# Kernel tuning notes

Measured on AMD Instinct MI355X. Metric: run time of the kernel, lower is better.

Reference implementation:

```python
import jax, jax.numpy as jnp
import numpy as np
from math import sqrt

NUM_HEADS = 8
HIDDEN = 768
ATTN_DIM = HIDDEN // NUM_HEADS  # 96
NEG = -1e10


def setup_inputs() -> dict:
    key = jax.random.key(0)
    ks = jax.random.split(key, 6)
    b, s, dim = 8, 1024, 768
    scale = 1.0 / sqrt(dim)
    return {
        "span_embeddings": jax.random.normal(ks[0], (b, s, dim), dtype=jnp.float32),
        "span_tags": jax.random.randint(ks[1], (b, s), 0, 5),
        "w_weight": jax.random.normal(ks[2], (1, dim), dtype=jnp.float32) * scale,
        "w_q": jax.random.normal(ks[3], (HIDDEN, dim), dtype=jnp.float32) * scale,
        "w_k": jax.random.normal(ks[4], (HIDDEN, dim), dtype=jnp.float32) * scale,
        "w_v": jax.random.normal(ks[5], (HIDDEN, dim), dtype=jnp.float32) * scale,
    }


def reference(span_embeddings, span_tags, w_weight, w_q, w_k, w_v):
    b, s, _ = span_embeddings.shape
    pad = span_tags == 0  # [b, s]

    # additive span attention weights: Linear(dim -> 1), mask padded, softmax over seq
    attn_weights = span_embeddings @ w_weight.T  # [b, s, 1]
    attn_weights = jnp.where(pad[:, :, None], NEG, attn_weights)
    attn_weights = jax.nn.softmax(attn_weights, axis=1)

    # NOTE: original views hidden as (attn_dim, num_heads) in that order
    qs = (span_embeddings @ w_q.T).reshape(b, s, ATTN_DIM, NUM_HEADS)
    ks = (span_embeddings @ w_k.T).reshape(b, s, ATTN_DIM, NUM_HEADS)
    vs = (span_embeddings @ w_v.T).reshape(b, s, ATTN_DIM, NUM_HEADS)

    rel = jnp.einsum('bqdh,bkdh->bqkh', qs, ks) / sqrt(ATTN_DIM)  # [b,q,k,h]
    # original masks along query axis (relevance_weights[span_tags.eq(0)] = NEG)
    rel = jnp.where(pad[:, :, None, None], NEG, rel)
    # original softmax(dim=-1) -> over the HEADS axis (faithful quirk)
    rel = jax.nn.softmax(rel, axis=-1)

    span_value = jnp.einsum('bqkh,bkdh->bqdh', rel, vs).reshape(b, s, HIDDEN)
    weighted_value = jnp.sum(attn_weights * span_value, axis=1)  # [b, hidden]
    return weighted_value
```

## Files before the change

kernel.cpp:

```cpp
#include <hip/hip_runtime.h>
#include <hip/hip_bf16.h>
#include <math.h>

#define NEGV (-1e10f)

typedef __attribute__((ext_vector_type(8))) short bf16x8;
typedef __attribute__((ext_vector_type(4))) float f32x4;
typedef __attribute__((ext_vector_type(16))) float f32x16;

static __device__ __forceinline__ unsigned short f2bf(float f) {
  unsigned int u = __builtin_bit_cast(unsigned int, f);
  unsigned int r = (u + 0x7fffu + ((u >> 16) & 1u)) >> 16;
  return (unsigned short)r;
}
static __device__ __forceinline__ float bf2f(unsigned short v) {
  return __builtin_bit_cast(float, (unsigned int)v << 16);
}

#define GLD16(g, l)                                                   \
  __builtin_amdgcn_global_load_lds(                                   \
      (const __attribute__((address_space(1))) void*)(g),             \
      (__attribute__((address_space(3))) void*)(l), 16, 0, 0)

__global__ __launch_bounds__(256) void cast_emb_logits(
    const float* __restrict__ emb, const int* __restrict__ tags,
    const float* __restrict__ ww, unsigned short* __restrict__ embbf,
    float* __restrict__ logits) {
  int w = threadIdx.x >> 6, lane = threadIdx.x & 63;
  int row = blockIdx.x * 4 + w;
  const float4* src = (const float4*)(emb + (size_t)row * 768);
  const float4* wsrc = (const float4*)ww;
  ushort4* dst = (ushort4*)(embbf + (size_t)row * 768);
  float d = 0.f;
#pragma unroll
  for (int j = 0; j < 3; j++) {
    int idx = lane + 64 * j;
    float4 v = src[idx];
    float4 wv = wsrc[idx];
    d += v.x * wv.x + v.y * wv.y + v.z * wv.z + v.w * wv.w;
    ushort4 o;
    o.x = f2bf(v.x); o.y = f2bf(v.y); o.z = f2bf(v.z); o.w = f2bf(v.w);
    dst[idx] = o;
  }
#pragma unroll
  for (int off = 32; off; off >>= 1) d += __shfl_xor(d, off);
  if (lane == 0) logits[row] = (tags[row] == 0) ? NEGV : d;
}

__global__ __launch_bounds__(256) void cast_w(
    const float* __restrict__ wq, const float* __restrict__ wk,
    const float* __restrict__ wv, unsigned short* __restrict__ out) {
  int z = blockIdx.y;
  const float* src = (z == 0) ? wq : (z == 1) ? wk : wv;
  int idx = blockIdx.x * 256 + threadIdx.x;
  float4 v = ((const float4*)src)[idx];
  ushort4 o;
  o.x = f2bf(v.x); o.y = f2bf(v.y); o.z = f2bf(v.z); o.w = f2bf(v.w);
  ((ushort4*)(out + (size_t)z * 589824))[idx] = o;
}

__global__ __launch_bounds__(256) void softmax_aw(
    const float* __restrict__ logits, float* __restrict__ aw) {
  __shared__ float red[4];
  int b = blockIdx.x, t = threadIdx.x;
  const float* L = logits + b * 1024;
  float x0 = L[t], x1 = L[t + 256], x2 = L[t + 512], x3 = L[t + 768];
  float m = fmaxf(fmaxf(x0, x1), fmaxf(x2, x3));
#pragma unroll
  for (int off = 32; off; off >>= 1) m = fmaxf(m, __shfl_xor(m, off));
  if ((t & 63) == 0) red[t >> 6] = m;
  __syncthreads();
  m = fmaxf(fmaxf(red[0], red[1]), fmaxf(red[2], red[3]));
  float e0 = __expf(x0 - m), e1 = __expf(x1 - m), e2 = __expf(x2 - m),
        e3 = __expf(x3 - m);
  float s = e0 + e1 + e2 + e3;
#pragma unroll
  for (int off = 32; off; off >>= 1) s += __shfl_xor(s, off);
  __syncthreads();
  if ((t & 63) == 0) red[t >> 6] = s;
  __syncthreads();
  float inv = 1.0f / (red[0] + red[1] + red[2] + red[3]);
  float* A = aw + b * 1024;
  A[t] = e0 * inv; A[t + 256] = e1 * inv;
  A[t + 512] = e2 * inv; A[t + 768] = e3 * inv;
}

__global__ __launch_bounds__(256) void qkv_gemm(
    const unsigned short* __restrict__ A, const unsigned short* __restrict__ Wbf,
    unsigned short* __restrict__ Qf, unsigned short* __restrict__ Kf,
    unsigned short* __restrict__ Vbf) {
  __shared__ __align__(16) unsigned short sm[16640];
  unsigned short* As = sm;
  unsigned short* Bs = sm + 8192;
  int z = blockIdx.z;
  const unsigned short* B = Wbf + (size_t)z * 589824;
  int mb = blockIdx.x * 128, nb = blockIdx.y * 128;
  int tid = threadIdx.x;
  int w = tid >> 6, lane = tid & 63;
  int wm = w >> 1, wn = w & 1;
  int c = lane & 15, quad = lane >> 4;
  int lrow = lane >> 2, lcol = (lane & 3) * 8;
  const unsigned short* Ag = A + (size_t)(mb + w * 32 + lrow) * 768 + lcol;
  const unsigned short* Bg = B + (size_t)(nb + w * 32 + lrow) * 768 + lcol;
  int woff = w * 1024;

#define PREFETCH(buf, kb)                                              \
  do {                                                                 \
    GLD16(Ag + (kb), As + (buf) * 4096 + woff);                        \
    GLD16(Ag + (kb) + 16 * 768, As + (buf) * 4096 + woff + 512);       \
    GLD16(Bg + (kb), Bs + (buf) * 4096 + woff);                        \
    GLD16(Bg + (kb) + 16 * 768, Bs + (buf) * 4096 + woff + 512);       \
  } while (0)

  f32x4 acc[4][4];
#pragma unroll
  for (int i = 0; i < 4; i++)
#pragma unroll
    for (int j = 0; j < 4; j++) acc[i][j] = 0;

  PREFETCH(0, 0);
  for (int it = 0; it < 24; it++) {
    __syncthreads();
    if (it + 1 < 24) PREFETCH((it + 1) & 1, (it + 1) * 32);
    const unsigned short* Ab = As + (it & 1) * 4096;
    const unsigned short* Bb = Bs + (it & 1) * 4096;
    bf16x8 af[4], bfr[4];
#pragma unroll
    for (int i = 0; i < 4; i++)
      af[i] = *(const bf16x8*)&Ab[(wm * 64 + i * 16 + c) * 32 + quad * 8];
#pragma unroll
    for (int j = 0; j < 4; j++)
      bfr[j] = *(const bf16x8*)&Bb[(wn * 64 + j * 16 + c) * 32 + quad * 8];
#pragma unroll
    for (int i = 0; i < 4; i++)
#pragma unroll
      for (int j = 0; j < 4; j++)
        acc[i][j] = __builtin_amdgcn_mfma_f32_16x16x32_bf16(af[i], bfr[j],
                                                            acc[i][j], 0, 0, 0);
  }
  __syncthreads();

  if (z == 2) {
#pragma unroll
    for (int i = 0; i < 4; i++)
#pragma unroll
      for (int j = 0; j < 4; j++)
#pragma unroll
        for (int r = 0; r < 4; r++) {
          int rowg = mb + wm * 64 + i * 16 + quad * 4 + r;
          int colg = nb + wn * 64 + j * 16 + c;
          Vbf[(size_t)rowg * 768 + colg] = f2bf(acc[i][j][r]);
        }
  } else {
    unsigned short* O = (z == 0) ? Qf : Kf;
#pragma unroll
    for (int i = 0; i < 4; i++) {
#pragma unroll
      for (int j = 0; j < 4; j++) {
#pragma unroll
        for (int r = 0; r < 4; r++) {
          int ql = wm * 64 + i * 16 + quad * 4 + r;
          int h = c & 7;
          int elem = j * 2 + (c >> 3);
          int chunkL = (ql >> 5) * 8 + h;
          int lane32 = (ql & 31) + wn * 32;
          sm[chunkL * 520 + lane32 * 8 + elem] = f2bf(acc[i][j][r]);
        }
      }
    }
    __syncthreads();
    int bq = mb >> 10;
    int qt32g0 = (mb & 1023) >> 5;
    int tt = blockIdx.y;
#pragma unroll
    for (int it2 = 0; it2 < 8; it2++) {
      int g = it2 * 256 + tid;
      int chunkL = g >> 6;
      int off = (g & 63) * 8;
      bf16x8 vdat = *(const bf16x8*)&sm[chunkL * 520 + off];
      int qt32 = qt32g0 + (chunkL >> 3), h = chunkL & 7;
      size_t dst = ((((size_t)(bq * 32 + qt32) * 8 + h) * 6 + tt) << 9) + off;
      *(bf16x8*)&O[dst] = vdat;
    }
  }
#undef PREFETCH
}

__global__ __launch_bounds__(256) void attn(
    const unsigned short* __restrict__ Qf, const unsigned short* __restrict__ Kf,
    const float* __restrict__ aw, float* __restrict__ Ptp) {
  __shared__ __align__(16) unsigned short Qs[2 * 6144];
  __shared__ __align__(16) unsigned short Ks[2 * 6144];
  __shared__ float pbuf[1024];
  int b = blockIdx.z, qb = blockIdx.y, kb = blockIdx.x;
  int tid = threadIdx.x, w = tid >> 6, lane = tid & 63;
  int wq = w >> 1, wk = w & 1;

#define STAGE(hh, buf)                                                        \
  do {                                                                        \
    _Pragma("unroll") for (int call = 0; call < 3; call++) {                  \
      int cc = call * 4 + w;                                                  \
      int qt32 = (cc >= 6) ? 1 : 0;                                           \
      int t5 = cc - qt32 * 6;                                                 \
      size_t go = ((((size_t)(b * 32 + qb * 2 + qt32) * 8 + (hh)) * 6 + t5)   \
                   << 9) + lane * 8;                                          \
      size_t ko = ((((size_t)(b * 32 + kb * 2 + qt32) * 8 + (hh)) * 6 + t5)   \
                   << 9) + lane * 8;                                          \
      GLD16(Qf + go, Qs + (buf) * 6144 + cc * 512);                           \
      GLD16(Kf + ko, Ks + (buf) * 6144 + cc * 512);                           \
    }                                                                         \
  } while (0)

  f32x16 acc[8];
#pragma unroll
  for (int h = 0; h < 8; h++) acc[h] = 0;

  STAGE(0, 0);
#pragma unroll
  for (int h = 0; h < 8; h++) {
    __syncthreads();
    if (h + 1 < 8) STAGE(h + 1, (h + 1) & 1);
    const unsigned short* Qb = Qs + (h & 1) * 6144;
    const unsigned short* Kb = Ks + (h & 1) * 6144;
#pragma unroll
    for (int t = 0; t < 6; t++) {
      bf16x8 a = *(const bf16x8*)&Qb[(wq * 6 + t) * 512 + lane * 8];
      bf16x8 bb = *(const bf16x8*)&Kb[(wk * 6 + t) * 512 + lane * 8];
      acc[h] = __builtin_amdgcn_mfma_f32_32x32x16_bf16(a, bb, acc[h], 0, 0, 0);
    }
  }

  float awv[16];
#pragma unroll
  for (int reg = 0; reg < 16; reg++) {
    int row = (reg & 3) + 8 * (reg >> 2) + 4 * (lane >> 5);
    awv[reg] = aw[b * 1024 + qb * 64 + wq * 32 + row];
  }
  float partial[8];
#pragma unroll
  for (int h = 0; h < 8; h++) partial[h] = 0.f;
  const float C2 = 0.10206207261596577f * 1.4426950408889634f;
#pragma unroll
  for (int reg = 0; reg < 16; reg++) {
    float v[8], m = -1e30f;
#pragma unroll
    for (int h = 0; h < 8; h++) {
      v[h] = acc[h][reg] * C2;
      m = fmaxf(m, v[h]);
    }
    float ssum = 0.f;
#pragma unroll
    for (int h = 0; h < 8; h++) {
      float e = exp2f(v[h] - m);
      v[h] = e;
      ssum += e;
    }
    float g = awv[reg] * __builtin_amdgcn_rcpf(ssum);
#pragma unroll
    for (int h = 0; h < 8; h++) partial[h] += v[h] * g;
  }
#pragma unroll
  for (int h = 0; h < 8; h++) {
    float v = partial[h];
    v += __shfl_xor(v, 32);
    partial[h] = v;
  }
  if (lane < 32) {
#pragma unroll
    for (int h = 0; h < 8; h++) pbuf[w * 256 + lane * 8 + h] = partial[h];
  }
  __syncthreads();
#pragma unroll
  for (int wk2 = 0; wk2 < 2; wk2++) {
    float s = pbuf[wk2 * 256 + tid] + pbuf[(2 + wk2) * 256 + tid];
    int kcol = tid >> 3, h = tid & 7;
    Ptp[(((size_t)qb * 8 + b) * 1024 + kb * 64 + wk2 * 32 + kcol) * 8 + h] = s;
  }
#undef STAGE
}

__global__ __launch_bounds__(256) void finalize(
    const float* __restrict__ Ptp, const unsigned short* __restrict__ Vbf,
    float* __restrict__ out) {
  __shared__ float ps[256];
  int kc = blockIdx.x, b = blockIdx.y;
  int t = threadIdx.x;
  {
    int k = kc * 32 + (t >> 3), h = t & 7;
    float s = 0.f;
#pragma unroll
    for (int qc = 0; qc < 16; qc++)
      s += Ptp[(((size_t)qc * 8 + b) * 1024 + k) * 8 + h];
    ps[t] = s;
  }
  __syncthreads();
  int h = t & 7;
  float a0 = 0, a1 = 0, a2 = 0;
  const unsigned short* Vb = Vbf + ((size_t)b * 1024 + kc * 32) * 768;
#pragma unroll 4
  for (int kk = 0; kk < 32; kk++) {
    float p = ps[kk * 8 + h];
    const unsigned short* vr = Vb + (size_t)kk * 768;
    a0 += p * bf2f(vr[t]);
    a1 += p * bf2f(vr[t + 256]);
    a2 += p * bf2f(vr[t + 512]);
  }
  atomicAdd(&out[b * 768 + t], a0);
  atomicAdd(&out[b * 768 + t + 256], a1);
  atomicAdd(&out[b * 768 + t + 512], a2);
}

extern "C" void kernel_launch(void* const* d_in, const int* in_sizes, int n_in,
                              void* d_out, int out_size, void* d_ws,
                              size_t ws_size, hipStream_t stream) {
  const float* emb = (const float*)d_in[0];
  const int* tags = (const int*)d_in[1];
  const float* ww = (const float*)d_in[2];
  const float* wq = (const float*)d_in[3];
  const float* wk = (const float*)d_in[4];
  const float* wv = (const float*)d_in[5];
  float* out = (float*)d_out;
  char* ws = (char*)d_ws;
  unsigned short* embbf = (unsigned short*)(ws + 0);
  unsigned short* wbf   = (unsigned short*)(ws + 12582912);
  unsigned short* Qf    = (unsigned short*)(ws + 16121856);
  unsigned short* Kf    = (unsigned short*)(ws + 28704768);
  unsigned short* Vbf   = (unsigned short*)(ws + 41287680);
  float* logits         = (float*)(ws + 53870592);
  float* aw             = (float*)(ws + 53903360);
  float* Ptp            = (float*)(ws + 53936128);

  hipMemsetAsync(out, 0, 8 * 768 * sizeof(float), stream);
  cast_emb_logits<<<2048, 256, 0, stream>>>(emb, tags, ww, embbf, logits);
  cast_w<<<dim3(576, 3), 256, 0, stream>>>(wq, wk, wv, wbf);
  softmax_aw<<<8, 256, 0, stream>>>(logits, aw);
  qkv_gemm<<<dim3(64, 6, 3), 256, 0, stream>>>(embbf, wbf, Qf, Kf, Vbf);
  attn<<<dim3(16, 16, 8), 256, 0, stream>>>(Qf, Kf, aw, Ptp);
  finalize<<<dim3(32, 8), 256, 0, stream>>>(Ptp, Vbf, out);
}
```

Measured before the change: 188.1 us.

## Merge cast kernels, load attn fragments directly from global, vectorize finalize

Merges the embedding cast/logit kernel and the weight cast kernel into a single launch that dispatches on block index, saving one launch. The attention kernel no longer stages Q/K through double-buffered LDS with barriers; each wave reads its MFMA fragments straight from the pre-tiled global layout, dropping the LDS footprint and syncs but losing cross-wave sharing (each Q/K tile is read twice from global/L2). The finalize kernel loads 4 bf16 values per thread with a vector load and uses 192 active threads instead of 256 doing scalar loads.

```diff
diff --git a/kernel.cpp b/kernel.cpp
--- a/kernel.cpp
+++ b/kernel.cpp
@@ -22,41 +22,43 @@
       (const __attribute__((address_space(1))) void*)(g),             \
       (__attribute__((address_space(3))) void*)(l), 16, 0, 0)
 
-__global__ __launch_bounds__(256) void cast_emb_logits(
+__global__ __launch_bounds__(256) void cast_inputs(
     const float* __restrict__ emb, const int* __restrict__ tags,
-    const float* __restrict__ ww, unsigned short* __restrict__ embbf,
-    float* __restrict__ logits) {
-  int w = threadIdx.x >> 6, lane = threadIdx.x & 63;
-  int row = blockIdx.x * 4 + w;
-  const float4* src = (const float4*)(emb + (size_t)row * 768);
-  const float4* wsrc = (const float4*)ww;
-  ushort4* dst = (ushort4*)(embbf + (size_t)row * 768);
-  float d = 0.f;
-#pragma unroll
-  for (int j = 0; j < 3; j++) {
-    int idx = lane + 64 * j;
-    float4 v = src[idx];
-    float4 wv = wsrc[idx];
-    d += v.x * wv.x + v.y * wv.y + v.z * wv.z + v.w * wv.w;
+    const float* __restrict__ ww, const float* __restrict__ wq,
+    const float* __restrict__ wk, const float* __restrict__ wv,
+    unsigned short* __restrict__ embbf, float* __restrict__ logits,
+    unsigned short* __restrict__ wbf) {
+  int bx = blockIdx.x;
+  if (bx < 2048) {
+    int w = threadIdx.x >> 6, lane = threadIdx.x & 63;
+    int row = bx * 4 + w;
+    const float4* src = (const float4*)(emb + (size_t)row * 768);
+    const float4* wsrc = (const float4*)ww;
+    ushort4* dst = (ushort4*)(embbf + (size_t)row * 768);
+    float d = 0.f;
+#pragma unroll
+    for (int j = 0; j < 3; j++) {
+      int idx = lane + 64 * j;
+      float4 v = src[idx];
+      float4 wv = wsrc[idx];
+      d += v.x * wv.x + v.y * wv.y + v.z * wv.z + v.w * wv.w;
+      ushort4 o;
+      o.x = f2bf(v.x); o.y = f2bf(v.y); o.z = f2bf(v.z); o.w = f2bf(v.w);
+      dst[idx] = o;
+    }
+#pragma unroll
+    for (int off = 32; off; off >>= 1) d += __shfl_xor(d, off);
+    if (lane == 0) logits[row] = (tags[row] == 0) ? NEGV : d;
+  } else {
+    int g = bx - 2048;
+    int z = g / 576;
+    int idx = (g - z * 576) * 256 + threadIdx.x;
+    const float* src = (z == 0) ? wq : (z == 1) ? wk : wv;
+    float4 v = ((const float4*)src)[idx];
     ushort4 o;
     o.x = f2bf(v.x); o.y = f2bf(v.y); o.z = f2bf(v.z); o.w = f2bf(v.w);
-    dst[idx] = o;
-  }
-#pragma unroll
-  for (int off = 32; off; off >>= 1) d += __shfl_xor(d, off);
-  if (lane == 0) logits[row] = (tags[row] == 0) ? NEGV : d;
-}
-
-__global__ __launch_bounds__(256) void cast_w(
-    const float* __restrict__ wq, const float* __restrict__ wk,
-    const float* __restrict__ wv, unsigned short* __restrict__ out) {
-  int z = blockIdx.y;
-  const float* src = (z == 0) ? wq : (z == 1) ? wk : wv;
-  int idx = blockIdx.x * 256 + threadIdx.x;
-  float4 v = ((const float4*)src)[idx];
-  ushort4 o;
-  o.x = f2bf(v.x); o.y = f2bf(v.y); o.z = f2bf(v.z); o.w = f2bf(v.w);
-  ((ushort4*)(out + (size_t)z * 589824))[idx] = o;
+    ((ushort4*)(wbf + (size_t)z * 589824))[idx] = o;
+  }
 }
 
 __global__ __launch_bounds__(256) void softmax_aw(
@@ -189,43 +191,24 @@
 __global__ __launch_bounds__(256) void attn(
     const unsigned short* __restrict__ Qf, const unsigned short* __restrict__ Kf,
     const float* __restrict__ aw, float* __restrict__ Ptp) {
-  __shared__ __align__(16) unsigned short Qs[2 * 6144];
-  __shared__ __align__(16) unsigned short Ks[2 * 6144];
   __shared__ float pbuf[1024];
   int b = blockIdx.z, qb = blockIdx.y, kb = blockIdx.x;
   int tid = threadIdx.x, w = tid >> 6, lane = tid & 63;
   int wq = w >> 1, wk = w & 1;
-
-#define STAGE(hh, buf)                                                        \
-  do {                                                                        \
-    _Pragma("unroll") for (int call = 0; call < 3; call++) {                  \
-      int cc = call * 4 + w;                                                  \
-      int qt32 = (cc >= 6) ? 1 : 0;                                           \
-      int t5 = cc - qt32 * 6;                                                 \
-      size_t go = ((((size_t)(b * 32 + qb * 2 + qt32) * 8 + (hh)) * 6 + t5)   \
-                   << 9) + lane * 8;                                          \
-      size_t ko = ((((size_t)(b * 32 + kb * 2 + qt32) * 8 + (hh)) * 6 + t5)   \
-                   << 9) + lane * 8;                                          \
-      GLD16(Qf + go, Qs + (buf) * 6144 + cc * 512);                           \
-      GLD16(Kf + ko, Ks + (buf) * 6144 + cc * 512);                           \
-    }                                                                         \
-  } while (0)
+  const unsigned short* Qb =
+      Qf + ((size_t)(b * 32 + qb * 2 + wq) * 48) * 512 + (size_t)lane * 8;
+  const unsigned short* Kb =
+      Kf + ((size_t)(b * 32 + kb * 2 + wk) * 48) * 512 + (size_t)lane * 8;
 
   f32x16 acc[8];
 #pragma unroll
   for (int h = 0; h < 8; h++) acc[h] = 0;
-
-  STAGE(0, 0);
 #pragma unroll
   for (int h = 0; h < 8; h++) {
-    __syncthreads();
-    if (h + 1 < 8) STAGE(h + 1, (h + 1) & 1);
-    const unsigned short* Qb = Qs + (h & 1) * 6144;
-    const unsigned short* Kb = Ks + (h & 1) * 6144;
 #pragma unroll
     for (int t = 0; t < 6; t++) {
-      bf16x8 a = *(const bf16x8*)&Qb[(wq * 6 + t) * 512 + lane * 8];
-      bf16x8 bb = *(const bf16x8*)&Kb[(wk * 6 + t) * 512 + lane * 8];
+      bf16x8 a = *(const bf16x8*)(Qb + (size_t)(h * 6 + t) * 512);
+      bf16x8 bb = *(const bf16x8*)(Kb + (size_t)(h * 6 + t) * 512);
       acc[h] = __builtin_amdgcn_mfma_f32_32x32x16_bf16(a, bb, acc[h], 0, 0, 0);
     }
   }
@@ -276,7 +259,6 @@
     int kcol = tid >> 3, h = tid & 7;
     Ptp[(((size_t)qb * 8 + b) * 1024 + kb * 64 + wk2 * 32 + kcol) * 8 + h] = s;
   }
-#undef STAGE
 }
 
 __global__ __launch_bounds__(256) void finalize(
@@ -294,20 +276,25 @@
     ps[t] = s;
   }
   __syncthreads();
-  int h = t & 7;
-  float a0 = 0, a1 = 0, a2 = 0;
-  const unsigned short* Vb = Vbf + ((size_t)b * 1024 + kc * 32) * 768;
+  if (t < 192) {
+    int o0 = t * 4;
+    int hb = o0 & 7;
+    float a0 = 0, a1 = 0, a2 = 0, a3 = 0;
+    const unsigned short* Vb = Vbf + ((size_t)b * 1024 + kc * 32) * 768 + o0;
 #pragma unroll 4
-  for (int kk = 0; kk < 32; kk++) {
-    float p = ps[kk * 8 + h];
-    const unsigned short* vr = Vb + (size_t)kk * 768;
-    a0 += p * bf2f(vr[t]);
-    a1 += p * bf2f(vr[t + 256]);
-    a2 += p * bf2f(vr[t + 512]);
-  }
-  atomicAdd(&out[b * 768 + t], a0);
-  atomicAdd(&out[b * 768 + t + 256], a1);
-  atomicAdd(&out[b * 768 + t + 512], a2);
+    for (int kk = 0; kk < 32; kk++) {
+      ushort4 vv = *(const ushort4*)(Vb + (size_t)kk * 768);
+      const float* p = &ps[kk * 8 + hb];
+      a0 += p[0] * bf2f(vv.x);
+      a1 += p[1] * bf2f(vv.y);
+      a2 += p[2] * bf2f(vv.z);
+      a3 += p[3] * bf2f(vv.w);
+    }
+    atomicAdd(&out[b * 768 + o0], a0);
+    atomicAdd(&out[b * 768 + o0 + 1], a1);
+    atomicAdd(&out[b * 768 + o0 + 2], a2);
+    atomicAdd(&out[b * 768 + o0 + 3], a3);
+  }
 }
 
 extern "C" void kernel_launch(void* const* d_in, const int* in_sizes, int n_in,
@@ -331,8 +318,8 @@
   float* Ptp            = (float*)(ws + 53936128);
 
   hipMemsetAsync(out, 0, 8 * 768 * sizeof(float), stream);
-  cast_emb_logits<<<2048, 256, 0, stream>>>(emb, tags, ww, embbf, logits);
-  cast_w<<<dim3(576, 3), 256, 0, stream>>>(wq, wk, wv, wbf);
+  cast_inputs<<<3776, 256, 0, stream>>>(emb, tags, ww, wq, wk, wv, embbf,
+                                        logits, wbf);
   softmax_aw<<<8, 256, 0, stream>>>(logits, aw);
   qkv_gemm<<<dim3(64, 6, 3), 256, 0, stream>>>(embbf, wbf, Qf, Kf, Vbf);
   attn<<<dim3(16, 16, 8), 256, 0, stream>>>(Qf, Kf, aw, Ptp);
```

Measured after the change: 179.1 us. 1.05x faster.
